# Kernel optimization log

Measured on AMD Instinct MI355X. Metric: run time of the kernel, lower is better.

## Reference

```python
import jax, jax.numpy as jnp
from jax import lax
import numpy as np

R, C = 1536, 1536


def setup_inputs() -> dict:
    key = jax.random.key(0)
    # binary mask: nonzero = foreground (gets a distance), zero = background
    mask = jax.random.randint(key, (R, C), 0, 2).astype(jnp.float32)
    return {"mask": mask}


def reference(mask):
    """Exact Euclidean distance transform, matching scipy.ndimage.distance_transform_edt.

    Two-phase separable (Meijster) algorithm:
      phase 1: per-column 1D distance (in rows) to nearest background pixel
      phase 2: per-row min-plus combine: D2[i,j] = min_k (g[i,k]^2 + (j-k)^2)
    Phase 2 is done as an exact vectorized min-plus against a [C,C] offset
    matrix, scanned over rows to bound memory.
    """
    n_rows, n_cols = mask.shape
    BIG = jnp.float32(n_rows + n_cols)  # > any achievable grid distance
    bg = (mask == 0)  # background => distance 0

    # ---- phase 1: vertical 1D distance per column ----
    def col_step(carry, row_bg):
        d = jnp.where(row_bg, jnp.float32(0.0), jnp.minimum(carry + 1.0, BIG))
        return d, d

    init = jnp.full((n_cols,), BIG, dtype=jnp.float32)
    _, down = lax.scan(col_step, init, bg)                 # top -> bottom
    _, up = lax.scan(col_step, init, bg, reverse=True)     # bottom -> top
    g = jnp.minimum(down, up)                              # [R, C]
    g2 = g * g

    # ---- phase 2: horizontal min-plus per row ----
    idx = jnp.arange(n_cols, dtype=jnp.float32)
    jk2 = (idx[:, None] - idx[None, :]) ** 2               # [C(j), C(k)]

    def row_step(_, g2_row):
        d2 = jnp.min(g2_row[None, :] + jk2, axis=1)        # [C]
        return None, d2

    _, d2 = lax.scan(row_step, None, g2)                   # [R, C]
    return jnp.sqrt(d2)
```

## Files before the change

### kernel.cpp

```cpp
#include <hip/hip_runtime.h>
#include <math.h>


#define RR 1536
#define CC 1536
#define BIGF 3072.0f
#define H   32
#define NCH 48

__global__ __launch_bounds__(256) void edt_sum(
    const float* __restrict__ mask,
    float* __restrict__ A,
    float* __restrict__ B)
{
    const int col = blockIdx.x * 256 + threadIdx.x;
    const int ch  = blockIdx.y;
    const float* __restrict__ p = mask + (size_t)(ch * H) * CC + col;
    float a = BIGF, b = BIGF;
    #pragma unroll
    for (int ri = 0; ri < H; ++ri) {
        bool bg = (p[ri * CC] == 0.0f);
        a = bg ? fminf(a, (float)ri) : a;
        b = bg ? (float)(H - 1 - ri) : b;
    }
    A[ch * CC + col] = a;
    B[ch * CC + col] = b;
}

__global__ __launch_bounds__(256) void edt_carry(
    const float* __restrict__ A,
    const float* __restrict__ B,
    float* __restrict__ CD,
    float* __restrict__ CU)
{
    const int tid = blockIdx.x * 256 + threadIdx.x;
    if (tid < CC) {
        const int col = tid;
        float carry = BIGF;
        for (int c = 0; c < NCH; ++c) {
            CD[c * CC + col] = carry;
            float b = B[c * CC + col];
            carry = (b < BIGF) ? b : fminf(carry + (float)H, BIGF);
        }
    } else if (tid < 2 * CC) {
        const int col = tid - CC;
        float carry = BIGF;
        for (int c = NCH - 1; c >= 0; --c) {
            CU[c * CC + col] = carry;
            float a = A[c * CC + col];
            carry = (a < BIGF) ? a : fminf(carry + (float)H, BIGF);
        }
    }
}

__global__ __launch_bounds__(256) void edt_fill(
    const float* __restrict__ mask,
    const float* __restrict__ CD,
    const float* __restrict__ CU,
    float* __restrict__ g2)
{
    const int col = blockIdx.x * 256 + threadIdx.x;
    const int ch  = blockIdx.y;
    const float* __restrict__ p = mask + (size_t)(ch * H) * CC + col;
    float d[H];
    float prev = CD[ch * CC + col];
    #pragma unroll
    for (int ri = 0; ri < H; ++ri) {
        float m = p[ri * CC];
        float dd = (m == 0.0f) ? 0.0f : fminf(prev + 1.0f, BIGF);
        d[ri] = dd;
        prev = dd;
    }
    float up = CU[ch * CC + col];
    float* __restrict__ q = g2 + (size_t)(ch * H) * CC + col;
    #pragma unroll
    for (int ri = H - 1; ri >= 0; --ri) {
        float u = (d[ri] == 0.0f) ? 0.0f : fminf(up + 1.0f, BIGF);
        up = u;
        float g = fminf(d[ri], u);
        q[ri * CC] = g * g;
    }
}

__global__ __launch_bounds__(256) void edt_hpass(
    const float* __restrict__ g2in,
    float* __restrict__ out)
{
    __shared__ float g2[CC];
    const int row = blockIdx.x;
    const int t = threadIdx.x;
    const float* __restrict__ grow = g2in + (size_t)row * CC;

    for (int c = t; c < CC; c += 256) g2[c] = grow[c];
    __syncthreads();

    float res[CC / 256];
    #pragma unroll
    for (int m = 0; m < CC / 256; ++m) {
        int j = t + m * 256;
        float best = g2[j];
        int dk = 1;
        while ((float)(dk * dk) < best) {
            float dk2 = (float)(dk * dk);
            int kl = j - dk;
            int kr = j + dk;
            bool any = false;
            if (kl >= 0)  { best = fminf(best, g2[kl] + dk2); any = true; }
            if (kr < CC)  { best = fminf(best, g2[kr] + dk2); any = true; }
            if (!any) break;
            ++dk;
        }
        res[m] = sqrtf(best);
    }

    float* __restrict__ orow = out + (size_t)row * CC;
    #pragma unroll
    for (int m = 0; m < CC / 256; ++m) orow[t + m * 256] = res[m];
}

extern "C" void kernel_launch(void* const* d_in, const int* in_sizes, int n_in,
                              void* d_out, int out_size, void* d_ws, size_t ws_size,
                              hipStream_t stream) {
    const float* mask = (const float*)d_in[0];
    float* out = (float*)d_out;

    float* A  = (float*)d_ws;
    float* B  = A  + NCH * CC;
    float* CD = B  + NCH * CC;
    float* CU = CD + NCH * CC;

    dim3 gridc(CC / 256, NCH);
    edt_sum  <<<gridc, 256, 0, stream>>>(mask, A, B);
    edt_carry<<<(2 * CC + 255) / 256, 256, 0, stream>>>(A, B, CD, CU);
    edt_fill <<<gridc, 256, 0, stream>>>(mask, CD, CU, out);
    edt_hpass<<<RR, 256, 0, stream>>>(out, out);
}
```

Baseline: 77.94 us.

## Fuse vertical fill and horizontal pass into per-strip kernel using packed bitmask

The mask is packed into per-column 6-bit background bitmasks, so the second full read of the float mask is replaced by a small bitmask read. The vertical fill and the horizontal min-plus pass are fused into one kernel: each block handles a 6-row strip and keeps g^2 in shared memory instead of writing it to global memory and reading it back. The chunk height drops from 32 to 6, so the serial carry kernel now walks 256 chunks per column instead of 48. That longer serial chain and the change to 512-thread blocks with larger shared memory could offset the saved traffic.

```diff
diff --git a/kernel.cpp b/kernel.cpp
--- a/kernel.cpp
+++ b/kernel.cpp
@@ -2,34 +2,29 @@
 #include <math.h>
 
 
-#define RR 1536
-#define CC 1536
+#define RR   1536
+#define CC   1536
 #define BIGF 3072.0f
-#define H   32
-#define NCH 48
+#define H    6
+#define NCH  256
 
 __global__ __launch_bounds__(256) void edt_sum(
     const float* __restrict__ mask,
-    float* __restrict__ A,
-    float* __restrict__ B)
+    unsigned* __restrict__ bits)
 {
     const int col = blockIdx.x * 256 + threadIdx.x;
     const int ch  = blockIdx.y;
     const float* __restrict__ p = mask + (size_t)(ch * H) * CC + col;
-    float a = BIGF, b = BIGF;
+    unsigned w = 0;
     #pragma unroll
     for (int ri = 0; ri < H; ++ri) {
-        bool bg = (p[ri * CC] == 0.0f);
-        a = bg ? fminf(a, (float)ri) : a;
-        b = bg ? (float)(H - 1 - ri) : b;
+        if (p[ri * CC] == 0.0f) w |= (1u << ri);
     }
-    A[ch * CC + col] = a;
-    B[ch * CC + col] = b;
+    bits[ch * CC + col] = w;
 }
 
 __global__ __launch_bounds__(256) void edt_carry(
-    const float* __restrict__ A,
-    const float* __restrict__ B,
+    const unsigned* __restrict__ bits,
     float* __restrict__ CD,
     float* __restrict__ CU)
 {
@@ -39,7 +34,9 @@
         float carry = BIGF;
         for (int c = 0; c < NCH; ++c) {
             CD[c * CC + col] = carry;
-            float b = B[c * CC + col];
+            unsigned w = bits[c * CC + col];
+            unsigned hb = 31u - __builtin_clz(w | 1u);
+            float b = w ? (float)(H - 1 - (int)hb) : BIGF;
             carry = (b < BIGF) ? b : fminf(carry + (float)H, BIGF);
         }
     } else if (tid < 2 * CC) {
@@ -47,75 +44,70 @@
         float carry = BIGF;
         for (int c = NCH - 1; c >= 0; --c) {
             CU[c * CC + col] = carry;
-            float a = A[c * CC + col];
+            unsigned w = bits[c * CC + col];
+            unsigned lb = __builtin_ctz(w | 0x80000000u);
+            float a = w ? (float)lb : BIGF;
             carry = (a < BIGF) ? a : fminf(carry + (float)H, BIGF);
         }
     }
 }
 
-__global__ __launch_bounds__(256) void edt_fill(
-    const float* __restrict__ mask,
+__global__ __launch_bounds__(512) void edt_strip(
+    const unsigned* __restrict__ bits,
     const float* __restrict__ CD,
     const float* __restrict__ CU,
-    float* __restrict__ g2)
-{
-    const int col = blockIdx.x * 256 + threadIdx.x;
-    const int ch  = blockIdx.y;
-    const float* __restrict__ p = mask + (size_t)(ch * H) * CC + col;
-    float d[H];
-    float prev = CD[ch * CC + col];
-    #pragma unroll
-    for (int ri = 0; ri < H; ++ri) {
-        float m = p[ri * CC];
-        float dd = (m == 0.0f) ? 0.0f : fminf(prev + 1.0f, BIGF);
-        d[ri] = dd;
-        prev = dd;
-    }
-    float up = CU[ch * CC + col];
-    float* __restrict__ q = g2 + (size_t)(ch * H) * CC + col;
-    #pragma unroll
-    for (int ri = H - 1; ri >= 0; --ri) {
-        float u = (d[ri] == 0.0f) ? 0.0f : fminf(up + 1.0f, BIGF);
-        up = u;
-        float g = fminf(d[ri], u);
-        q[ri * CC] = g * g;
-    }
-}
-
-__global__ __launch_bounds__(256) void edt_hpass(
-    const float* __restrict__ g2in,
     float* __restrict__ out)
 {
-    __shared__ float g2[CC];
-    const int row = blockIdx.x;
-    const int t = threadIdx.x;
-    const float* __restrict__ grow = g2in + (size_t)row * CC;
+    __shared__ float g2[H][CC];
+    const int ch = blockIdx.x;
+    const int t  = threadIdx.x;
 
-    for (int c = t; c < CC; c += 256) g2[c] = grow[c];
+    #pragma unroll
+    for (int m = 0; m < CC / 512; ++m) {
+        const int c = t + m * 512;
+        const unsigned w = bits[ch * CC + c];
+        float d[H];
+        float prev = CD[ch * CC + c];
+        #pragma unroll
+        for (int ri = 0; ri < H; ++ri) {
+            bool bg = (w >> ri) & 1u;
+            float dd = bg ? 0.0f : fminf(prev + 1.0f, BIGF);
+            d[ri] = dd;
+            prev = dd;
+        }
+        float up = CU[ch * CC + c];
+        #pragma unroll
+        for (int ri = H - 1; ri >= 0; --ri) {
+            bool bg = (w >> ri) & 1u;
+            float u = bg ? 0.0f : fminf(up + 1.0f, BIGF);
+            up = u;
+            float g = fminf(d[ri], u);
+            g2[ri][c] = g * g;
+        }
+    }
     __syncthreads();
 
-    float res[CC / 256];
+    float* __restrict__ obase = out + (size_t)(ch * H) * CC;
     #pragma unroll
-    for (int m = 0; m < CC / 256; ++m) {
-        int j = t + m * 256;
-        float best = g2[j];
-        int dk = 1;
-        while ((float)(dk * dk) < best) {
-            float dk2 = (float)(dk * dk);
-            int kl = j - dk;
-            int kr = j + dk;
-            bool any = false;
-            if (kl >= 0)  { best = fminf(best, g2[kl] + dk2); any = true; }
-            if (kr < CC)  { best = fminf(best, g2[kr] + dk2); any = true; }
-            if (!any) break;
-            ++dk;
+    for (int r = 0; r < H; ++r) {
+        #pragma unroll
+        for (int m = 0; m < CC / 512; ++m) {
+            const int j = t + m * 512;
+            float best = g2[r][j];
+            int dk = 1;
+            while ((float)(dk * dk) < best) {
+                float dk2 = (float)(dk * dk);
+                int kl = j - dk;
+                int kr = j + dk;
+                bool any = false;
+                if (kl >= 0)  { best = fminf(best, g2[r][kl] + dk2); any = true; }
+                if (kr < CC)  { best = fminf(best, g2[r][kr] + dk2); any = true; }
+                if (!any) break;
+                ++dk;
+            }
+            obase[r * CC + j] = sqrtf(best);
         }
-        res[m] = sqrtf(best);
     }
-
-    float* __restrict__ orow = out + (size_t)row * CC;
-    #pragma unroll
-    for (int m = 0; m < CC / 256; ++m) orow[t + m * 256] = res[m];
 }
 
 extern "C" void kernel_launch(void* const* d_in, const int* in_sizes, int n_in,
@@ -124,14 +116,11 @@
     const float* mask = (const float*)d_in[0];
     float* out = (float*)d_out;
 
-    float* A  = (float*)d_ws;
-    float* B  = A  + NCH * CC;
-    float* CD = B  + NCH * CC;
+    unsigned* bits = (unsigned*)d_ws;
+    float* CD = (float*)(bits + NCH * CC);
     float* CU = CD + NCH * CC;
 
-    dim3 gridc(CC / 256, NCH);
-    edt_sum  <<<gridc, 256, 0, stream>>>(mask, A, B);
-    edt_carry<<<(2 * CC + 255) / 256, 256, 0, stream>>>(A, B, CD, CU);
-    edt_fill <<<gridc, 256, 0, stream>>>(mask, CD, CU, out);
-    edt_hpass<<<RR, 256, 0, stream>>>(out, out);
+    edt_sum  <<<dim3(CC / 256, NCH), 256, 0, stream>>>(mask, bits);
+    edt_carry<<<(2 * CC + 255) / 256, 256, 0, stream>>>(bits, CD, CU);
+    edt_strip<<<NCH, 512, 0, stream>>>(bits, CD, CU, out);
 }
```

New measurement: 100.0 us. 28.3% more time.
